# Performance work log

Hardware: AMD Instinct MI355X
Metric: run time of the kernel (lower is better)

The kernel has to match this reference:

```python
import jax, jax.numpy as jnp
import numpy as np
from jax import lax

D_MODEL, D_STATE, DT_RANK, D_INNER, K = 96, 16, 6, 192, 4


def cross_scan(x):
    # x: (B, C, H, W) -> (B, 4, C, L)
    B, C, H, W = x.shape
    x0 = x.reshape(B, C, H * W)                         # row-major scan
    x1 = jnp.transpose(x, (0, 1, 3, 2)).reshape(B, C, H * W)  # column-major scan
    return jnp.stack([x0, x1, x0[..., ::-1], x1[..., ::-1]], axis=1)


def cross_merge(ys, H, W):
    # ys: (B, 4, D, L) -> (B, D, L)
    B, Kd, D, L = ys.shape
    ys = ys[:, 0:2] + ys[:, 2:4, :, ::-1]
    y1 = jnp.transpose(ys[:, 1].reshape(B, D, W, H), (0, 1, 3, 2)).reshape(B, D, L)
    return ys[:, 0] + y1


def selective_scan(u, delta, A, Bs, Cs, Ds, delta_bias):
    # u, delta: (B, K, D, L); A: (K, D, N); Bs, Cs: (B, K, N, L); Ds, delta_bias: (K, D)
    Bsz, Kd, Dm, L = u.shape
    N = A.shape[-1]
    delta = jax.nn.softplus(delta + delta_bias[None, :, :, None])
    du = delta * u
    d_l = jnp.moveaxis(delta, -1, 0)   # (L, B, K, D)
    du_l = jnp.moveaxis(du, -1, 0)
    b_l = jnp.moveaxis(Bs, -1, 0)      # (L, B, K, N)
    c_l = jnpp = jnp.moveaxis(Cs, -1, 0)

    def step(h, inp):
        d_t, du_t, b_t, c_t = inp
        h = jnp.exp(d_t[..., None] * A) * h + du_t[..., None] * b_t[:, :, None, :]
        y = jnp.einsum('bkdn,bkn->bkd', h, c_t)
        return h, y

    h0 = jnp.zeros((Bsz, Kd, Dm, N), u.dtype)
    _, ys = lax.scan(step, h0, (d_l, du_l, b_l, c_l))
    ys = jnp.moveaxis(ys, 0, -1)  # (B, K, D, L)
    return ys + Ds[None, :, :, None] * u


def _forward(x, in_proj_w, conv_w, conv_b, x_proj_w, dt_projs_w, dt_projs_b,
             A_logs, Ds, out_norm_w, out_norm_b, out_proj_w):
    Bsz, H, W, dm = x.shape
    d_in = conv_w.shape[0]
    R, N = dt_projs_w.shape[2], A_logs.shape[-1]
    L = H * W
    # in_proj (no bias), split into x and gate z
    xz = jnp.einsum('bhwc,oc->bhwo', x, in_proj_w)
    xpart, z = jnp.split(xz, 2, axis=-1)
    z = jax.nn.silu(z)
    # depthwise 3x3 conv (NCHW) + SiLU
    xc = jnp.transpose(xpart, (0, 3, 1, 2))
    xc = lax.conv_general_dilated(xc, conv_w, (1, 1), 'SAME',
                                  feature_group_count=d_in,
                                  dimension_numbers=('NCHW', 'OIHW', 'NCHW'))
    xc = jax.nn.silu(xc + conv_b[None, :, None, None])
    # 4-directional cross scan
    xs = cross_scan(xc)                                   # (B, 4, d_in, L)
    x_dbl = jnp.einsum('bkdl,kcd->bkcl', xs, x_proj_w)    # (B, 4, R+2N, L)
    dts = jnp.einsum('bkrl,kdr->bkdl', x_dbl[:, :, :R], dt_projs_w)
    Bs = x_dbl[:, :, R:R + N]
    Cs = x_dbl[:, :, R + N:]
    A = -jnp.exp(A_logs)                                  # (4, d_in, N)
    ys = selective_scan(xs, dts, A, Bs, Cs, Ds, dt_projs_b)
    y = cross_merge(ys, H, W)                             # (B, d_in, L)
    y = jnp.transpose(y.reshape(Bsz, d_in, H, W), (0, 2, 3, 1))
    # out_norm = LayerNorm(d_inner), eps=1e-5
    mu = y.mean(-1, keepdims=True)
    var = ((y - mu) ** 2).mean(-1, keepdims=True)
    y = (y - mu) / jnp.sqrt(var + 1e-5) * out_norm_w + out_norm_b
    y = y * z
    return jnp.einsum('bhwd,od->bhwo', y, out_proj_w)


def setup_inputs() -> dict:
    key = jax.random.key(0)
    ks = jax.random.split(key, 8)
    dm, d_in, N, R = D_MODEL, D_INNER, D_STATE, DT_RANK
    x = jax.random.normal(ks[0], (8, 64, 64, dm), jnp.float32)
    in_proj_w = jax.random.normal(ks[1], (2 * d_in, dm), jnp.float32) * 0.02
    conv_w = jax.random.normal(ks[2], (d_in, 1, 3, 3), jnp.float32) * 0.1
    conv_b = jnp.zeros((d_in,), jnp.float32)
    x_proj_w = jax.random.normal(ks[3], (K, R + 2 * N, d_in), jnp.float32) * 0.02
    dt_projs_w = jax.random.normal(ks[4], (K, d_in, R), jnp.float32) * 0.1
    dt_projs_b = jax.random.uniform(ks[5], (K, d_in), jnp.float32, minval=-4.0, maxval=-2.0)
    A_logs = jnp.log(jnp.tile(jnp.arange(1, N + 1, dtype=jnp.float32)[None, None, :], (K, d_in, 1)))
    Ds = jnp.ones((K, d_in), jnp.float32)
    out_norm_w = jnp.ones((d_in,), jnp.float32)
    out_norm_b = jnp.zeros((d_in,), jnp.float32)
    out_proj_w = jax.random.normal(ks[6], (dm, d_in), jnp.float32) * 0.02
    return dict(x=x, in_proj_w=in_proj_w, conv_w=conv_w, conv_b=conv_b,
                x_proj_w=x_proj_w, dt_projs_w=dt_projs_w, dt_projs_b=dt_projs_b,
                A_logs=A_logs, Ds=Ds, out_norm_w=out_norm_w, out_norm_b=out_norm_b,
                out_proj_w=out_proj_w)


def reference(x, in_proj_w, conv_w, conv_b, x_proj_w, dt_projs_w, dt_projs_b,
              A_logs, Ds, out_norm_w, out_norm_b, out_proj_w):
    return _forward(x, in_proj_w, conv_w, conv_b, x_proj_w, dt_projs_w, dt_projs_b,
                    A_logs, Ds, out_norm_w, out_norm_b, out_proj_w)
```

## Files before the change

kernel.cpp:

```cpp
#include <hip/hip_runtime.h>
#include <math.h>

#define B_SZ 8
#define Hh 64
#define Ww 64
#define L 4096
#define Dm 96
#define Din 192
#define Kd 4
#define Ns 16
#define CPROJ 38
#define ROWW 40
#define NCHUNK 128
#define CHUNK 32

__device__ __forceinline__ float siluf_(float x){ return x / (1.f + __expf(-x)); }

__global__ void prep_kernel(const float* __restrict__ inw,
                            const float* __restrict__ xpw,
                            const float* __restrict__ outw,
                            float* __restrict__ wt_in,
                            float* __restrict__ wt_x,
                            float* __restrict__ wt_out){
  int i = blockIdx.x * blockDim.x + threadIdx.x;
  if (i < Dm*2*Din){ int k = i/(2*Din); int o = i%(2*Din); wt_in[i] = inw[o*Dm + k]; }
  int j = i - Dm*2*Din;
  if (j >= 0 && j < Din*Kd*CPROJ){ int k = j/(Kd*CPROJ); int c = j%(Kd*CPROJ); wt_x[j] = xpw[c*Din + k]; }
  int l = j - Din*Kd*CPROJ;
  if (l >= 0 && l < Din*Dm){ int dd = l/Dm; int o = l%Dm; wt_out[l] = outw[o*Din + dd]; }
}

__global__ __launch_bounds__(256) void zero_kernel(float4* __restrict__ p, int n4){
  int i = blockIdx.x * 256 + threadIdx.x;
  if (i < n4) p[i] = make_float4(0.f,0.f,0.f,0.f);
}

template<int KDIM, int OREAL, int EPI>
__global__ __launch_bounds__(256) void gemm_kernel(const float* __restrict__ X,
    const float* __restrict__ W, float* __restrict__ out0, float* __restrict__ out1){
  __shared__ float4 xt[128*24];
  const int tid = threadIdx.x;
  const int pg = tid & 15, og = tid >> 4;
  const int pblk = blockIdx.x & 255;
  const int oblk = blockIdx.x >> 8;
  const int p0 = pblk * 128;
  const bool act = (oblk*128 + og*8) < OREAL;
  int oc = oblk*128 + og*8;
  if (oc > OREAL-8) oc = OREAL-8;
  const int sw = pg & 7;

  float acc[8][8];
  #pragma unroll
  for (int i=0;i<8;i++){
    #pragma unroll
    for (int j2=0;j2<8;j2++) acc[i][j2] = 0.f;
  }

  for (int kp = 0; kp < KDIM/96; ++kp){
    __syncthreads();
    for (int idx = tid; idx < 128*24; idx += 256){
      int pp = idx/24, k4 = idx%24;
      size_t prow = (size_t)p0 + pp;
      float4 v = *(const float4*)&X[prow*KDIM + (size_t)kp*96 + k4*4];
      xt[pp*24 + (k4 ^ (pp&7))] = v;
    }
    __syncthreads();

    if (act){
      for (int k4 = 0; k4 < 24; ++k4){
        float4 wv[8];
        #pragma unroll
        for (int kk=0;kk<4;kk++){
          const float* wr = &W[(size_t)(kp*96 + k4*4 + kk)*OREAL + oc];
          wv[kk*2]   = *(const float4*)wr;
          wv[kk*2+1] = *(const float4*)(wr+4);
        }
        float4 xv[8];
        #pragma unroll
        for (int i=0;i<8;i++) xv[i] = xt[(pg+16*i)*24 + (k4 ^ sw)];
        #pragma unroll
        for (int kk=0;kk<4;kk++){
          const float4 wa = wv[kk*2], wb = wv[kk*2+1];
          #pragma unroll
          for (int i=0;i<8;i++){
            const float xk = ((const float*)&xv[i])[kk];
            acc[i][0] += xk*wa.x; acc[i][1] += xk*wa.y; acc[i][2] += xk*wa.z; acc[i][3] += xk*wa.w;
            acc[i][4] += xk*wb.x; acc[i][5] += xk*wb.y; acc[i][6] += xk*wb.z; acc[i][7] += xk*wb.w;
          }
        }
      }
    }
  }

  if (!act) return;
  if (EPI == 0){
    #pragma unroll
    for (int i=0;i<8;i++){
      size_t p = (size_t)p0 + pg + 16*i;
      if (oc < Din){
        *(float4*)&out0[p*Din + oc]     = make_float4(acc[i][0],acc[i][1],acc[i][2],acc[i][3]);
        *(float4*)&out0[p*Din + oc + 4] = make_float4(acc[i][4],acc[i][5],acc[i][6],acc[i][7]);
      } else {
        int zo = oc - Din;
        *(float4*)&out1[p*Din + zo]     = make_float4(siluf_(acc[i][0]),siluf_(acc[i][1]),siluf_(acc[i][2]),siluf_(acc[i][3]));
        *(float4*)&out1[p*Din + zo + 4] = make_float4(siluf_(acc[i][4]),siluf_(acc[i][5]),siluf_(acc[i][6]),siluf_(acc[i][7]));
      }
    }
  } else {
    #pragma unroll
    for (int i=0;i<8;i++){
      const int p = p0 + pg + 16*i;
      const int b = p >> 12;
      const int hw = p & (L-1);
      #pragma unroll
      for (int j2=0;j2<8;j2++){
        int c = oc + j2;
        int kd = c / CPROJ; int cc = c - kd*CPROJ;
        int dcol = (cc < 6) ? (32+cc) : (cc-6);
        out0[((size_t)(b*Kd+kd)*L + hw)*ROWW + dcol] = acc[i][j2];
      }
    }
  }
}

__global__ __launch_bounds__(256) void conv_kernel(const float* __restrict__ xp,
    const float* __restrict__ cw, const float* __restrict__ cb, float* __restrict__ u){
  const int gid = blockIdx.x * 256 + threadIdx.x;
  const int d = gid % Din; const int p = gid / Din;
  const int b = p / L; const int hw = p % L; const int h = hw >> 6; const int w = hw & 63;
  float acc = cb[d];
  #pragma unroll
  for (int i=-1;i<=1;i++){
    const int hh = h + i; if (hh < 0 || hh >= Hh) continue;
    #pragma unroll
    for (int j=-1;j<=1;j++){
      const int ww = w + j; if (ww < 0 || ww >= Ww) continue;
      acc += xp[((size_t)(b*L + hh*Ww + ww))*Din + d] * cw[d*9 + (i+1)*3 + (j+1)];
    }
  }
  u[(size_t)p*Din + d] = siluf_(acc);
}

__device__ __forceinline__ void affine_pos(int k, int t0, int& gp0, int& gstr){
  if (k == 0){ gp0 = t0; gstr = 1; }
  else if (k == 1){ gp0 = ((t0 & 63) << 6) | (t0 >> 6); gstr = 64; }
  else if (k == 2){ gp0 = L-1-t0; gstr = -1; }
  else { const int T0 = L-1-t0; gp0 = ((T0 & 63) << 6) | (T0 >> 6); gstr = -64; }
}

__device__ __forceinline__ void ladder_(float e1, float* e){
  e[0]=e1;
  #pragma unroll
  for (int n=1;n<16;n++){ int P=n+1; e[n] = e[(P+1)/2 - 1] * e[P/2 - 1]; }
}

__global__ __launch_bounds__(192) void scan_local_kernel(const float* __restrict__ u,
    const float* __restrict__ xq, const float* __restrict__ dtw,
    const float* __restrict__ dtb, const float* __restrict__ alog,
    const float* __restrict__ Dsin,
    float* __restrict__ qout, float* __restrict__ Sout, float* __restrict__ ym){
  const int bid = blockIdx.x;
  const int c = bid & (NCHUNK-1); const int k = (bid >> 7) & 3; const int b = bid >> 9;
  const int d = threadIdx.x;
  const int bk = b*Kd + k;
  float wdt[6];
  #pragma unroll
  for (int r=0;r<6;r++) wdt[r] = dtw[(k*Din + d)*6 + r];
  const float bias = dtb[k*Din + d];
  const float Dval = Dsin[k*Din + d];
  float a2[16]; bool fastb = true;
  #pragma unroll
  for (int n=0;n<16;n++){
    a2[n] = -__expf(alog[(k*Din + d)*16 + n]);
    fastb = fastb && (fabsf(a2[n] + (float)(n+1)) < 1e-5f*(float)(n+1));
  }
  const bool fast = (bool)__all((int)fastb);
  float h[16];
  #pragma unroll
  for (int n=0;n<16;n++) h[n] = 0.f;
  float S = 0.f;
  const int t0 = c * CHUNK;
  int gp0, gstr; affine_pos(k, t0, gp0, gstr);
  const float* __restrict__ up = u + (size_t)b*L*Din + (size_t)gp0*Din + d;
  float* __restrict__ yp = ym + (size_t)b*L*Din + (size_t)gp0*Din + d;
  const ptrdiff_t ustep = (ptrdiff_t)gstr * Din;
  const float* __restrict__ rowp = xq + ((size_t)bk*L + gp0)*ROWW;
  const ptrdiff_t rstep = (ptrdiff_t)gstr * ROWW;
  #pragma unroll 4
  for (int s = 0; s < CHUNK; ++s){
    const float4* __restrict__ rq = (const float4*)rowp;
    const float4 B0=rq[0],B1=rq[1],B2=rq[2],B3=rq[3];
    const float4 C0=rq[4],C1=rq[5],C2=rq[6],C3=rq[7];
    const float4 D0=rq[8];
    const float2 D1=((const float2*)rowp)[18];
    const float uval = *up;
    float dr = bias + D0.x*wdt[0]+D0.y*wdt[1]+D0.z*wdt[2]+D0.w*wdt[3]+D1.x*wdt[4]+D1.y*wdt[5];
    const float pp = __expf(dr);
    const float delta = (dr > 20.f) ? dr : __logf(1.f + pp);
    S += delta;
    const float du = delta * uval;
    float e[16];
    if (fast){
      ladder_(__builtin_amdgcn_rcpf(1.f + pp), e);
    } else {
      #pragma unroll
      for (int n=0;n<16;n++) e[n] = __expf(delta * a2[n]);
    }
    h[0] =e[0] *h[0] +du*B0.x; h[1] =e[1] *h[1] +du*B0.y; h[2] =e[2] *h[2] +du*B0.z; h[3] =e[3] *h[3] +du*B0.w;
    h[4] =e[4] *h[4] +du*B1.x; h[5] =e[5] *h[5] +du*B1.y; h[6] =e[6] *h[6] +du*B1.z; h[7] =e[7] *h[7] +du*B1.w;
    h[8] =e[8] *h[8] +du*B2.x; h[9] =e[9] *h[9] +du*B2.y; h[10]=e[10]*h[10]+du*B2.z; h[11]=e[11]*h[11]+du*B2.w;
    h[12]=e[12]*h[12]+du*B3.x; h[13]=e[13]*h[13]+du*B3.y; h[14]=e[14]*h[14]+du*B3.z; h[15]=e[15]*h[15]+du*B3.w;
    float y0 = h[0]*C0.x + h[1]*C0.y;  float y1 = h[2]*C0.z + h[3]*C0.w;
    float y2 = h[4]*C1.x + h[5]*C1.y;  float y3 = h[6]*C1.z + h[7]*C1.w;
    y0 += h[8]*C2.x + h[9]*C2.y;   y1 += h[10]*C2.z + h[11]*C2.w;
    y2 += h[12]*C3.x + h[13]*C3.y; y3 += h[14]*C3.z + h[15]*C3.w;
    atomicAdd(yp, (y0+y1)+(y2+y3) + Dval*uval);
    up += ustep; yp += ustep; rowp += rstep;
  }
  const size_t base = ((size_t)bk*NCHUNK + c)*Ns*Din + d;
  #pragma unroll
  for (int n=0;n<16;n++) qout[base + (size_t)n*Din] = h[n];
  Sout[((size_t)bk*NCHUNK + c)*Din + d] = S;
}

__global__ __launch_bounds__(256) void combine_kernel(const float* __restrict__ alog,
    const float* __restrict__ qin, const float* __restrict__ Sin, float* __restrict__ hout){
  const int gid = blockIdx.x * 256 + threadIdx.x;
  if (gid >= B_SZ*Kd*Ns*Din) return;
  const int d = gid % Din; const int n = (gid / Din) % Ns; const int bk = gid / (Din*Ns);
  const int k = bk & 3;
  const float A = -__expf(alog[(k*Din + d)*16 + n]);
  const size_t stepQ = (size_t)Ns*Din;
  size_t idx = ((size_t)bk*NCHUNK)*stepQ + (size_t)n*Din + d;
  size_t sidx = ((size_t)bk*NCHUNK)*Din + d;
  float h = 0.f;
  for (int c0=0;c0<NCHUNK;c0+=8){
    float qv[8], Sv[8];
    #pragma unroll
    for (int j=0;j<8;j++){ qv[j] = qin[idx + (size_t)j*stepQ]; Sv[j] = Sin[sidx + (size_t)j*Din]; }
    #pragma unroll
    for (int j=0;j<8;j++){
      hout[idx + (size_t)j*stepQ] = h;
      h = __expf(A*Sv[j])*h + qv[j];
    }
    idx += 8*stepQ; sidx += (size_t)8*Din;
  }
}

__global__ __launch_bounds__(192) void scan_corr_kernel(const float* __restrict__ xq,
    const float* __restrict__ dtw, const float* __restrict__ dtb,
    const float* __restrict__ alog, const float* __restrict__ hin,
    float* __restrict__ ym){
  const int bid = blockIdx.x;
  const int c = bid & (NCHUNK-1); const int k = (bid >> 7) & 3; const int b = bid >> 9;
  const int d = threadIdx.x;
  const int bk = b*Kd + k;
  float wdt[6];
  #pragma unroll
  for (int r=0;r<6;r++) wdt[r] = dtw[(k*Din + d)*6 + r];
  const float bias = dtb[k*Din + d];
  float a2[16]; bool fastb = true;
  #pragma unroll
  for (int n=0;n<16;n++){
    a2[n] = -__expf(alog[(k*Din + d)*16 + n]);
    fastb = fastb && (fabsf(a2[n] + (float)(n+1)) < 1e-5f*(float)(n+1));
  }
  const bool fast = (bool)__all((int)fastb);
  float g[16];
  const size_t hbase = ((size_t)bk*NCHUNK + c)*Ns*Din + d;
  #pragma unroll
  for (int n=0;n<16;n++) g[n] = hin[hbase + (size_t)n*Din];

  const int t0 = c * CHUNK;
  int gp0, gstr; affine_pos(k, t0, gp0, gstr);
  float* __restrict__ yp = ym + (size_t)b*L*Din + (size_t)gp0*Din + d;
  const ptrdiff_t ustep = (ptrdiff_t)gstr * Din;
  const float* __restrict__ rowp = xq + ((size_t)bk*L + gp0)*ROWW;
  const ptrdiff_t rstep = (ptrdiff_t)gstr * ROWW;
  float E = 1.f, cumS = 0.f;
  #pragma unroll 4
  for (int s = 0; s < CHUNK; ++s){
    const float4* __restrict__ rq = (const float4*)rowp;
    const float4 C0=rq[4],C1=rq[5],C2=rq[6],C3=rq[7];
    const float4 D0=rq[8];
    const float2 D1=((const float2*)rowp)[18];
    float dr = bias + D0.x*wdt[0]+D0.y*wdt[1]+D0.z*wdt[2]+D0.w*wdt[3]+D1.x*wdt[4]+D1.y*wdt[5];
    const float pp = __expf(dr);
    float lad[16];
    if (fast){
      E *= __builtin_amdgcn_rcpf(1.f + pp);
      ladder_(E, lad);
    } else {
      const float delta = (dr > 20.f) ? dr : __logf(1.f + pp);
      cumS += delta;
      #pragma unroll
      for (int n=0;n<16;n++) lad[n] = __expf(a2[n]*cumS);
    }
    float w0[16];
    #pragma unroll
    for (int n=0;n<16;n++) w0[n] = lad[n]*g[n];
    float y0 = w0[0]*C0.x + w0[1]*C0.y;  float y1 = w0[2]*C0.z + w0[3]*C0.w;
    float y2 = w0[4]*C1.x + w0[5]*C1.y;  float y3 = w0[6]*C1.z + w0[7]*C1.w;
    y0 += w0[8]*C2.x + w0[9]*C2.y;   y1 += w0[10]*C2.z + w0[11]*C2.w;
    y2 += w0[12]*C3.x + w0[13]*C3.y; y3 += w0[14]*C3.z + w0[15]*C3.w;
    atomicAdd(yp, (y0+y1)+(y2+y3));
    yp += ustep; rowp += rstep;
  }
}

__global__ __launch_bounds__(192) void outproj_kernel(const float* __restrict__ ym,
    const float* __restrict__ z, const float* __restrict__ gw, const float* __restrict__ gb,
    const float* __restrict__ wto,
    float* __restrict__ out){
  __shared__ float xt[64*192];
  __shared__ float smu[64], sinv[64];
  const int tid = threadIdx.x;
  const int p0 = blockIdx.x * 64;
  if (tid < 128){
    const int r = tid >> 1, part = tid & 1;
    const float4* __restrict__ src = (const float4*)(ym + (size_t)(p0 + r)*Din + part*96);
    float s = 0.f, ss = 0.f;
    #pragma unroll
    for (int i=0;i<24;i++){
      float4 v = src[i];
      s  += (v.x+v.y)+(v.z+v.w);
      ss += (v.x*v.x+v.y*v.y)+(v.z*v.z+v.w*v.w);
    }
    s += __shfl_xor(s, 1); ss += __shfl_xor(ss, 1);
    if (!part){
      const float mu = s * (1.f/Din);
      smu[r] = mu;
      sinv[r] = rsqrtf(ss*(1.f/Din) - mu*mu + 1e-5f);
    }
  }
  __syncthreads();
  for (int idx = tid; idx < 64*48; idx += 192){
    const int r = idx/48, k4 = idx - (idx/48)*48;
    const size_t g = (size_t)(p0+r)*Din + k4*4;
    float4 v  = *(const float4*)(ym + g);
    const float4 zv = *(const float4*)(z + g);
    const float4 gwv = *(const float4*)(gw + k4*4);
    const float4 gbv = *(const float4*)(gb + k4*4);
    const float mu = smu[r], inv = sinv[r];
    v.x = ((v.x-mu)*inv*gwv.x + gbv.x)*zv.x;
    v.y = ((v.y-mu)*inv*gwv.y + gbv.y)*zv.y;
    v.z = ((v.z-mu)*inv*gwv.z + gbv.z)*zv.z;
    v.w = ((v.w-mu)*inv*gwv.w + gbv.w)*zv.w;
    const int k4s = (k4 & ~7) | ((k4 ^ r) & 7);
    *(float4*)(xt + r*192 + k4s*4) = v;
  }
  __syncthreads();
  const int pg = tid/12, og = tid - (tid/12)*12;
  const int oc = og*8;
  float acc[4][8];
  #pragma unroll
  for (int i=0;i<4;i++){
    #pragma unroll
    for (int j=0;j<8;j++) acc[i][j] = 0.f;
  }
  for (int k4 = 0; k4 < 48; ++k4){
    float4 xv[4];
    #pragma unroll
    for (int i=0;i<4;i++){
      const int r = pg*4+i;
      const int k4s = (k4 & ~7) | ((k4 ^ r) & 7);
      xv[i] = *(const float4*)(xt + r*192 + k4s*4);
    }
    #pragma unroll
    for (int j=0;j<4;j++){
      const int k = k4*4 + j;
      const float4 w0 = *(const float4*)(wto + (size_t)k*Dm + oc);
      const float4 w1 = *(const float4*)(wto + (size_t)k*Dm + oc + 4);
      #pragma unroll
      for (int i=0;i<4;i++){
        const float xk = ((const float*)&xv[i])[j];
        acc[i][0] += xk*w0.x; acc[i][1] += xk*w0.y; acc[i][2] += xk*w0.z; acc[i][3] += xk*w0.w;
        acc[i][4] += xk*w1.x; acc[i][5] += xk*w1.y; acc[i][6] += xk*w1.z; acc[i][7] += xk*w1.w;
      }
    }
  }
  #pragma unroll
  for (int i=0;i<4;i++){
    const size_t row = (size_t)p0 + pg*4 + i;
    *(float4*)(out + row*Dm + oc)     = make_float4(acc[i][0],acc[i][1],acc[i][2],acc[i][3]);
    *(float4*)(out + row*Dm + oc + 4) = make_float4(acc[i][4],acc[i][5],acc[i][6],acc[i][7]);
  }
}

extern "C" void kernel_launch(void* const* d_in, const int* in_sizes, int n_in,
                              void* d_out, int out_size, void* d_ws, size_t ws_size,
                              hipStream_t stream) {
  const float* x      = (const float*)d_in[0];
  const float* inw    = (const float*)d_in[1];
  const float* convw  = (const float*)d_in[2];
  const float* convb  = (const float*)d_in[3];
  const float* xprojw = (const float*)d_in[4];
  const float* dtw    = (const float*)d_in[5];
  const float* dtb    = (const float*)d_in[6];
  const float* alog   = (const float*)d_in[7];
  const float* Ds     = (const float*)d_in[8];
  const float* gw     = (const float*)d_in[9];
  const float* gb     = (const float*)d_in[10];
  const float* outw   = (const float*)d_in[11];
  float* out = (float*)d_out;

  float* ws = (float*)d_ws;
  const size_t nBLD  = (size_t)B_SZ*L*Din;
  const size_t nXQ   = (size_t)B_SZ*Kd*L*ROWW;
  const size_t nQ    = (size_t)B_SZ*Kd*NCHUNK*Ns*Din;
  const size_t nS    = (size_t)B_SZ*Kd*NCHUNK*Din;
  size_t off = 0;
  float* xpart = ws + off; off += nQ;
  float* zbuf  = ws + off; off += nBLD;
  float* ubuf  = ws + off; off += nBLD;
  float* xq    = ws + off; off += nXQ;
  float* qbuf  = ws + off; off += nQ;
  float* Sbuf  = ws + off; off += nS;
  float* ym    = ws + off; off += nBLD;
  float* wt_in = ws + off; off += (size_t)Dm*2*Din;
  float* wt_x  = ws + off; off += (size_t)Din*Kd*CPROJ;
  float* wt_out= ws + off; off += (size_t)Din*Dm;

  const int prepN = Dm*2*Din + Din*Kd*CPROJ + Din*Dm;
  prep_kernel<<<(prepN + 255)/256, 256, 0, stream>>>(inw, xprojw, outw, wt_in, wt_x, wt_out);
  zero_kernel<<<(int)(nBLD/4 + 255)/256, 256, 0, stream>>>((float4*)ym, (int)(nBLD/4));
  gemm_kernel<Dm, 2*Din, 0><<<256*3, 256, 0, stream>>>(x, wt_in, xpart, zbuf);
  conv_kernel<<<(int)(nBLD/256), 256, 0, stream>>>(xpart, convw, convb, ubuf);
  gemm_kernel<Din, Kd*CPROJ, 1><<<256*2, 256, 0, stream>>>(ubuf, wt_x, xq, nullptr);
  scan_local_kernel<<<B_SZ*Kd*NCHUNK, Din, 0, stream>>>(ubuf, xq, dtw, dtb, alog, Ds, qbuf, Sbuf, ym);
  combine_kernel<<<(B_SZ*Kd*Ns*Din + 255)/256, 256, 0, stream>>>(alog, qbuf, Sbuf, xpart);
  scan_corr_kernel<<<B_SZ*Kd*NCHUNK, Din, 0, stream>>>(xq, dtw, dtb, alog, xpart, ym);
  outproj_kernel<<<B_SZ*L/64, 192, 0, stream>>>(ym, zbuf, gw, gb, wt_out, out);
}
```

Baseline: 455.9 us.

## Vectorize conv with transposed weights, fuse ym zeroing, pad x_proj output columns

The depthwise conv now works on four channels per thread with float4 loads from a transposed weight table built in the prep kernel. The ym zeroing is folded into the conv kernel, which removes one launch. The x_proj weights are padded and reordered to 40 columns per direction so the GEMM epilogue can write contiguous float4s instead of scattered scalar stores. The cost is slightly more padded GEMM work.

Result: faster. 413.8 us (-9.2%).

```diff
diff --git a/kernel.cpp b/kernel.cpp
--- a/kernel.cpp
+++ b/kernel.cpp
@@ -11,6 +11,7 @@
 #define Ns 16
 #define CPROJ 38
 #define ROWW 40
+#define XCOLS 160
 #define NCHUNK 128
 #define CHUNK 32
 
@@ -19,20 +20,28 @@
 __global__ void prep_kernel(const float* __restrict__ inw,
                             const float* __restrict__ xpw,
                             const float* __restrict__ outw,
+                            const float* __restrict__ convw,
                             float* __restrict__ wt_in,
                             float* __restrict__ wt_x,
-                            float* __restrict__ wt_out){
+                            float* __restrict__ wt_out,
+                            float* __restrict__ cwt){
   int i = blockIdx.x * blockDim.x + threadIdx.x;
   if (i < Dm*2*Din){ int k = i/(2*Din); int o = i%(2*Din); wt_in[i] = inw[o*Dm + k]; }
   int j = i - Dm*2*Din;
-  if (j >= 0 && j < Din*Kd*CPROJ){ int k = j/(Kd*CPROJ); int c = j%(Kd*CPROJ); wt_x[j] = xpw[c*Din + k]; }
-  int l = j - Din*Kd*CPROJ;
+  if (j >= 0 && j < Din*XCOLS){
+    int k = j/XCOLS; int c = j%XCOLS;
+    int kd = c/ROWW; int dcol = c%ROWW;
+    float v = 0.f;
+    if (dcol < 38){
+      int cc = (dcol < 32) ? (dcol + 6) : (dcol - 32);
+      v = xpw[(kd*CPROJ + cc)*Din + k];
+    }
+    wt_x[j] = v;
+  }
+  int l = j - Din*XCOLS;
   if (l >= 0 && l < Din*Dm){ int dd = l/Dm; int o = l%Dm; wt_out[l] = outw[o*Din + dd]; }
-}
-
-__global__ __launch_bounds__(256) void zero_kernel(float4* __restrict__ p, int n4){
-  int i = blockIdx.x * 256 + threadIdx.x;
-  if (i < n4) p[i] = make_float4(0.f,0.f,0.f,0.f);
+  int m = l - Din*Dm;
+  if (m >= 0 && m < 9*Din){ int widx = m/Din; int d = m%Din; cwt[m] = convw[d*9 + widx]; }
 }
 
 template<int KDIM, int OREAL, int EPI>
@@ -107,38 +116,41 @@
       }
     }
   } else {
+    const int kd = oc / ROWW;
+    const int dcol = oc - kd*ROWW;
     #pragma unroll
     for (int i=0;i<8;i++){
       const int p = p0 + pg + 16*i;
       const int b = p >> 12;
       const int hw = p & (L-1);
-      #pragma unroll
-      for (int j2=0;j2<8;j2++){
-        int c = oc + j2;
-        int kd = c / CPROJ; int cc = c - kd*CPROJ;
-        int dcol = (cc < 6) ? (32+cc) : (cc-6);
-        out0[((size_t)(b*Kd+kd)*L + hw)*ROWW + dcol] = acc[i][j2];
-      }
+      float* dst = &out0[((size_t)(b*Kd+kd)*L + hw)*ROWW + dcol];
+      *(float4*)dst       = make_float4(acc[i][0],acc[i][1],acc[i][2],acc[i][3]);
+      *(float4*)(dst + 4) = make_float4(acc[i][4],acc[i][5],acc[i][6],acc[i][7]);
     }
   }
 }
 
 __global__ __launch_bounds__(256) void conv_kernel(const float* __restrict__ xp,
-    const float* __restrict__ cw, const float* __restrict__ cb, float* __restrict__ u){
+    const float* __restrict__ cwt, const float* __restrict__ cb,
+    float* __restrict__ u, float4* __restrict__ ymz){
   const int gid = blockIdx.x * 256 + threadIdx.x;
-  const int d = gid % Din; const int p = gid / Din;
-  const int b = p / L; const int hw = p % L; const int h = hw >> 6; const int w = hw & 63;
-  float acc = cb[d];
+  ymz[gid] = make_float4(0.f,0.f,0.f,0.f);
+  const int p = gid / 48; const int d0 = (gid - p*48)*4;
+  const int b = p >> 12; const int hw = p & (L-1); const int h = hw >> 6; const int w = hw & 63;
+  float4 acc = *(const float4*)&cb[d0];
   #pragma unroll
   for (int i=-1;i<=1;i++){
     const int hh = h + i; if (hh < 0 || hh >= Hh) continue;
     #pragma unroll
     for (int j=-1;j<=1;j++){
       const int ww = w + j; if (ww < 0 || ww >= Ww) continue;
-      acc += xp[((size_t)(b*L + hh*Ww + ww))*Din + d] * cw[d*9 + (i+1)*3 + (j+1)];
-    }
-  }
-  u[(size_t)p*Din + d] = siluf_(acc);
+      const float4 xv = *(const float4*)&xp[((size_t)(b*L + hh*Ww + ww))*Din + d0];
+      const float4 wv = *(const float4*)&cwt[((i+1)*3 + (j+1))*Din + d0];
+      acc.x += xv.x*wv.x; acc.y += xv.y*wv.y; acc.z += xv.z*wv.z; acc.w += xv.w*wv.w;
+    }
+  }
+  acc.x = siluf_(acc.x); acc.y = siluf_(acc.y); acc.z = siluf_(acc.z); acc.w = siluf_(acc.w);
+  *(float4*)&u[(size_t)p*Din + d0] = acc;
 }
 
 __device__ __forceinline__ void affine_pos(int k, int t0, int& gp0, int& gstr){
@@ -418,15 +430,16 @@
   float* Sbuf  = ws + off; off += nS;
   float* ym    = ws + off; off += nBLD;
   float* wt_in = ws + off; off += (size_t)Dm*2*Din;
-  float* wt_x  = ws + off; off += (size_t)Din*Kd*CPROJ;
+  float* wt_x  = ws + off; off += (size_t)Din*XCOLS;
   float* wt_out= ws + off; off += (size_t)Din*Dm;
-
-  const int prepN = Dm*2*Din + Din*Kd*CPROJ + Din*Dm;
-  prep_kernel<<<(prepN + 255)/256, 256, 0, stream>>>(inw, xprojw, outw, wt_in, wt_x, wt_out);
-  zero_kernel<<<(int)(nBLD/4 + 255)/256, 256, 0, stream>>>((float4*)ym, (int)(nBLD/4));
+  float* cwt   = ws + off; off += (size_t)9*Din;
+
+  const int prepN = Dm*2*Din + Din*XCOLS + Din*Dm + 9*Din;
+  prep_kernel<<<(prepN + 255)/256, 256, 0, stream>>>(inw, xprojw, outw, convw,
+                                                     wt_in, wt_x, wt_out, cwt);
   gemm_kernel<Dm, 2*Din, 0><<<256*3, 256, 0, stream>>>(x, wt_in, xpart, zbuf);
-  conv_kernel<<<(int)(nBLD/256), 256, 0, stream>>>(xpart, convw, convb, ubuf);
-  gemm_kernel<Din, Kd*CPROJ, 1><<<256*2, 256, 0, stream>>>(ubuf, wt_x, xq, nullptr);
+  conv_kernel<<<(int)(nBLD/4/256), 256, 0, stream>>>(xpart, cwt, convb, ubuf, (float4*)ym);
+  gemm_kernel<Din, XCOLS, 1><<<256*2, 256, 0, stream>>>(ubuf, wt_x, xq, nullptr);
   scan_local_kernel<<<B_SZ*Kd*NCHUNK, Din, 0, stream>>>(ubuf, xq, dtw, dtb, alog, Ds, qbuf, Sbuf, ym);
   combine_kernel<<<(B_SZ*Kd*Ns*Din + 255)/256, 256, 0, stream>>>(alog, qbuf, Sbuf, xpart);
   scan_corr_kernel<<<B_SZ*Kd*NCHUNK, Din, 0, stream>>>(xq, dtw, dtb, alog, xpart, ym);
```
